# Kernel tuning notes

Measured on AMD Instinct MI355X. Metric: run time of the kernel, lower is better.

The kernel has to match this reference:

```python
import jax, jax.numpy as jnp
import numpy as np
from jax import lax

B, S, D, T = 64, 256, 1024, 60
HIST = 20  # last-20 window of attn / decoder-state history


def setup_inputs() -> dict:
    key = jax.random.key(0)
    ks = jax.random.split(key, 8)
    e_outputs = jax.random.normal(ks[0], (B, S, D), jnp.float32)
    queries = jax.random.normal(ks[1], (B, T, D), jnp.float32)
    # attention weights over source frames: rows sum to 1
    attns = jax.nn.softmax(jax.random.normal(ks[2], (B, T, S), jnp.float32), axis=-1)
    g = 0.02
    Wr = jax.random.normal(ks[3], (D, 1), jnp.float32) * g
    br = jnp.zeros((1,), jnp.float32)
    Wa = jax.random.normal(ks[4], (D, 1), jnp.float32) * g
    ba = jnp.zeros((1,), jnp.float32)
    Wq = jax.random.normal(ks[5], (D, D), jnp.float32) / np.sqrt(D)
    Wn = jax.random.normal(ks[6], (2 * D, 1), jnp.float32) * g
    bn = jnp.zeros((1,), jnp.float32)
    return {"e_outputs": e_outputs, "queries": queries, "attns": attns,
            "Wr": Wr, "br": br, "Wa": Wa, "ba": ba, "Wq": Wq, "Wn": Wn, "bn": bn}


def reference(e_outputs, queries, attns, Wr, br, Wa, ba, Wq, Wn, bn):
    Bn, Sn, Dn = e_outputs.shape
    # decay1[i] = (i+1)/20 ; decay2[i] = 1-(i+1)/50, zero-padded past 50 frames
    decay1 = (jnp.arange(HIST, dtype=jnp.float32) + 1.0) / 20.0
    idx = jnp.arange(Sn, dtype=jnp.float32)
    add0 = jnp.where(idx < 50, 1.0 - (idx + 1.0) / 50.0, 0.0)
    add_state0 = add0[None, :, None]                       # [1,S,1]
    mem0 = e_outputs * add_state0                          # [B,S,D]
    abuf0 = jnp.zeros((HIST, Bn, Sn), e_outputs.dtype)
    qbuf0 = jnp.zeros((HIST, Bn, Dn), e_outputs.dtype)

    def step(carry, x):
        mem, add_state, abuf, qbuf, i = carry
        attn_i, q_i = x                                    # [B,S], [B,D]
        # read: selected frame before memory update
        sel = jnp.einsum('bs,bsd->bd', attn_i, mem)
        # roll history buffers (newest at slot HIST-1)
        abuf = jnp.concatenate([abuf[1:], attn_i[None]], axis=0)
        qbuf = jnp.concatenate([qbuf[1:], q_i[None]], axis=0)
        k = jnp.minimum(i + 1, HIST)
        valid = jnp.arange(HIST) >= (HIST - k)
        temp = jax.nn.softmax(jnp.where(valid, decay1, -jnp.inf))
        attn_w = jnp.einsum('t,tbs->bs', temp, abuf)       # decayed attn sum
        query_s = jnp.einsum('t,tbd->bd', temp, qbuf)      # decayed query sum
        remove_prob = jax.nn.sigmoid(q_i @ Wr + br)[:, :, None]   # [B,1,1]
        add_prob = jax.nn.sigmoid(q_i @ Wa + ba)[:, :, None]      # [B,1,1]
        sim = jax.nn.sigmoid(jnp.einsum('bsd,bd->bs', mem, query_s @ Wq))[..., None]
        mem = mem * (1.0 - remove_prob * attn_w[..., None] * sim)
        last_ctx = jnp.einsum('bs,bsd->bd', attn_w, e_outputs)[:, None, :]
        cat = jnp.concatenate([e_outputs, jnp.broadcast_to(last_ctx, e_outputs.shape)], axis=-1)
        nxt = jax.nn.sigmoid(cat @ Wn + bn)                # [B,S,1]
        mem = mem + e_outputs * (1.0 - add_state) * (add_prob * nxt)
        add_state = add_state + (1.0 - add_state) * (add_prob * nxt)
        return (mem, add_state, abuf, qbuf, i + 1), sel

    init = (mem0, jnp.broadcast_to(add_state0, (Bn, Sn, 1)), abuf0, qbuf0, jnp.int32(0))
    xs = (attns.transpose(1, 0, 2), queries.transpose(1, 0, 2))
    _, sels = lax.scan(step, init, xs)
    return sels.transpose(1, 0, 2)                         # [B,T,D]
```

## Files before the change

### kernel.cpp

```cpp
#include <hip/hip_runtime.h>
#include <math.h>


#define Bn 64
#define Sn 256
#define Dn 1024
#define Tn 60
#define HISTn 20
#define LDK 72
#define K05 1.0512710963760241f
#define EINV 0.36787944117144233f

typedef __bf16 bf16x8 __attribute__((ext_vector_type(8)));
typedef float f32x4 __attribute__((ext_vector_type(4)));
typedef unsigned short us8 __attribute__((ext_vector_type(8)));

typedef const __attribute__((address_space(1))) unsigned int* gas_u32p;
typedef __attribute__((address_space(3))) unsigned int* las_u32p;

__device__ __forceinline__ void gl16(const unsigned short* g, unsigned short* l){
  __builtin_amdgcn_global_load_lds((gas_u32p)g, (las_u32p)l, 16, 0, 0);
}

__device__ __forceinline__ unsigned short f2bf(float f){
  unsigned int x; __builtin_memcpy(&x,&f,4);
  unsigned int lsb = (x >> 16) & 1u;
  x += 0x7fffu + lsb;
  return (unsigned short)(x >> 16);
}
__device__ __forceinline__ float sigmoidf_(float x){ return 1.0f/(1.0f+expf(-x)); }

__global__ __launch_bounds__(256) void conv_fused(
    const float* __restrict__ Q, const float* __restrict__ Wr,
    const float* __restrict__ br, const float* __restrict__ Wa,
    const float* __restrict__ ba, const float* __restrict__ Wq,
    const float* __restrict__ E, const float* __restrict__ Wn,
    float* __restrict__ rp, float* __restrict__ ap,
    unsigned short* __restrict__ Qbf, unsigned short* __restrict__ WT,
    unsigned short* __restrict__ Ebf,
    float* __restrict__ eW1, float* __restrict__ eW2)
{
  int tid = threadIdx.x;
  int bx = blockIdx.x;
  if (bx < Bn*Tn){
    int row = bx;
    float4 x = ((const float4*)(Q + (size_t)row*Dn))[tid];
    float4 a = ((const float4*)Wr)[tid];
    float4 b = ((const float4*)Wa)[tid];
    unsigned short o[4] = {f2bf(x.x), f2bf(x.y), f2bf(x.z), f2bf(x.w)};
    *(uint2*)&Qbf[(size_t)row*Dn + tid*4] = *(uint2*)o;
    float s1 = x.x*a.x + x.y*a.y + x.z*a.z + x.w*a.w;
    float s2 = x.x*b.x + x.y*b.y + x.z*b.z + x.w*b.w;
    for (int off = 32; off; off >>= 1){
      s1 += __shfl_down(s1, off, 64);
      s2 += __shfl_down(s2, off, 64);
    }
    __shared__ float r1[4], r2[4];
    int lane = tid & 63, wv = tid >> 6;
    if (lane == 0){ r1[wv] = s1; r2[wv] = s2; }
    __syncthreads();
    if (tid == 0){
      rp[row] = sigmoidf_(r1[0]+r1[1]+r1[2]+r1[3] + br[0]);
      ap[row] = sigmoidf_(r2[0]+r2[1]+r2[2]+r2[3] + ba[0]);
    }
  } else if (bx < Bn*Tn + 256){
    __shared__ __align__(16) unsigned short Tt[64][LDK];
    int t = bx - Bn*Tn;
    int n0 = (t >> 4)*64, k0 = (t & 15)*64;
    int kl = tid >> 4, nl4 = (tid & 15)*4;
    #pragma unroll
    for (int it = 0; it < 4; it++){
      int k = kl + it*16;
      float4 v = *(const float4*)&Wq[(size_t)(k0+k)*Dn + n0 + nl4];
      Tt[nl4+0][k] = f2bf(v.x); Tt[nl4+1][k] = f2bf(v.y);
      Tt[nl4+2][k] = f2bf(v.z); Tt[nl4+3][k] = f2bf(v.w);
    }
    __syncthreads();
    int nr = tid >> 2, kg = (tid & 3)*16;
    *(us8*)&WT[(size_t)(n0+nr)*Dn + k0+kg]   = *(us8*)&Tt[nr][kg];
    *(us8*)&WT[(size_t)(n0+nr)*Dn + k0+kg+8] = *(us8*)&Tt[nr][kg+8];
  } else {
    int row = (bx - (Bn*Tn + 256))*4 + (tid >> 6);
    int lane = tid & 63;
    const float* er = E + (size_t)row*Dn;
    unsigned short* ebr = Ebf + (size_t)row*Dn;
    float d1 = 0.f, d2 = 0.f;
    #pragma unroll
    for (int c = 0; c < 4; c++){
      int idx = c*64 + lane;
      float4 v = ((const float4*)er)[idx];
      float4 w1 = ((const float4*)Wn)[idx];
      float4 w2 = ((const float4*)(Wn + Dn))[idx];
      unsigned short o[4] = {f2bf(v.x), f2bf(v.y), f2bf(v.z), f2bf(v.w)};
      ((uint2*)ebr)[idx] = *(uint2*)o;
      d1 += v.x*w1.x + v.y*w1.y + v.z*w1.z + v.w*w1.w;
      d2 += v.x*w2.x + v.y*w2.y + v.z*w2.z + v.w*w2.w;
    }
    #pragma unroll
    for (int off = 32; off; off >>= 1){
      d1 += __shfl_down(d1, off, 64);
      d2 += __shfl_down(d2, off, 64);
    }
    if (lane == 0){ eW1[row] = d1; eW2[row] = d2; }
  }
}

__global__ __launch_bounds__(256) void gemm_qw_kr(
    const unsigned short* __restrict__ Qbf,
    const unsigned short* __restrict__ WT,
    const float* __restrict__ At,
    const float* __restrict__ eW2,
    unsigned short* __restrict__ QWbf,
    float* __restrict__ lc)
{
  int tid = threadIdx.x;
  if (blockIdx.x < (Bn*Tn/64)*(Dn/64)){
    __shared__ __align__(16) unsigned short As[64*64], Bs[64*64];
    int bx = blockIdx.x;
    int m0 = (bx >> 4) * 64, n0 = (bx & 15) * 64;
    int lane = tid & 63, wave = tid >> 6;
    int quad = lane >> 4, l16 = lane & 15;
    f32x4 acc[4];
    #pragma unroll
    for (int nt=0;nt<4;nt++)
      #pragma unroll
      for (int r=0;r<4;r++) acc[nt][r]=0.f;
    int c0 = wave*2;
    int srow = c0*8 + (lane >> 3);
    int scol = ((lane & 7) ^ (lane >> 3)) * 8;
    const unsigned short* gA0 = Qbf + (size_t)(m0 + srow)*Dn + scol;
    const unsigned short* gA1 = gA0 + 8*Dn;
    const unsigned short* gB0 = WT  + (size_t)(n0 + srow)*Dn + scol;
    const unsigned short* gB1 = gB0 + 8*Dn;
    unsigned short* lA0 = &As[c0*512];
    unsigned short* lA1 = &As[c0*512 + 512];
    unsigned short* lB0 = &Bs[c0*512];
    unsigned short* lB1 = &Bs[c0*512 + 512];
    int mrow = wave*16 + l16;
    for (int k0 = 0; k0 < Dn; k0 += 64){
      gl16(gA0 + k0, lA0);
      gl16(gA1 + k0, lA1);
      gl16(gB0 + k0, lB0);
      gl16(gB1 + k0, lB1);
      __syncthreads();
      #pragma unroll
      for (int kk = 0; kk < 2; kk++){
        bf16x8 a = *(const bf16x8*)&As[ mrow*64 + ((kk*32 + quad*8) ^ ((mrow&7)*8)) ];
        #pragma unroll
        for (int nt=0;nt<4;nt++){
          int nrow = nt*16 + l16;
          bf16x8 bb = *(const bf16x8*)&Bs[ nrow*64 + ((kk*32 + quad*8) ^ ((nrow&7)*8)) ];
          acc[nt] = __builtin_amdgcn_mfma_f32_16x16x32_bf16(a, bb, acc[nt], 0, 0, 0);
        }
      }
      __syncthreads();
    }
    #pragma unroll
    for (int nt=0;nt<4;nt++)
      #pragma unroll
      for (int r=0;r<4;r++){
        int m = m0 + wave*16 + quad*4 + r;
        int n = n0 + nt*16 + l16;
        QWbf[(size_t)m*Dn + n] = f2bf(acc[nt][r]);
      }
  } else {
    int b = blockIdx.x - (Bn*Tn/64)*(Dn/64);
    int lane = tid & 63, wv = tid >> 6;
    __shared__ float Rsh[Tn];
    float4 e2v = ((const float4*)(eW2 + (size_t)b*Sn))[lane];
    const float* at_b = At + (size_t)b*Tn*Sn;
    #pragma unroll
    for (int w = 0; w < 15; w++){
      int j = wv + w*4;
      float4 a4 = ((const float4*)(at_b + (size_t)j*Sn))[lane];
      float v = a4.x*e2v.x + a4.y*e2v.y + a4.z*e2v.z + a4.w*e2v.w;
      #pragma unroll
      for (int off = 32; off; off >>= 1) v += __shfl_down(v, off, 64);
      if (lane == 0) Rsh[j] = v;
    }
    __syncthreads();
    if (tid < Tn){
      int i = tid;
      int j0 = (i - HISTn + 1 > 0) ? i - HISTn + 1 : 0;
      float num = 0.f, den = 0.f;
      float wj = 1.f;
      for (int j = 0; j <= i; j++){
        wj *= K05;
        if (j >= j0){ num += wj * Rsh[j]; den += wj; }
      }
      lc[b*Tn + i] = num / den;
    }
  }
}

__global__ __launch_bounds__(256) void g_scan(
    const unsigned short* __restrict__ QWbf,
    const unsigned short* __restrict__ Ebf,
    const float* __restrict__ At,
    const float* __restrict__ rp,
    const float* __restrict__ ap,
    const float* __restrict__ eW1,
    const float* __restrict__ lc,
    const float* __restrict__ bnp,
    unsigned short* __restrict__ Pbf)
{
  __shared__ __align__(16) unsigned short As[64][LDK], Bs[64][LDK];
  __shared__ __align__(16) float AtL[Tn][64], GL[Tn][64];
  __shared__ float lcs[Tn], rps[Tn], aps[Tn];
  int b = blockIdx.x, s0 = blockIdx.y * 64;
  int tid = threadIdx.x, lane = tid & 63, wave = tid >> 6;
  int quad = lane >> 4, l16 = lane & 15;

  const float* at_b = At + (size_t)b*Tn*Sn + s0;
  #pragma unroll
  for (int it = 0; it < 4; it++){
    int r = it*16 + (tid >> 4);
    if (r < Tn){
      int c4 = (tid & 15)*4;
      *(float4*)&AtL[r][c4] = *(const float4*)&at_b[(size_t)r*Sn + c4];
    }
  }
  if (tid < Tn){
    lcs[tid] = lc[b*Tn + tid];
    rps[tid] = rp[b*Tn + tid];
    aps[tid] = ap[b*Tn + tid];
  }

  f32x4 acc[4];
  #pragma unroll
  for (int nt=0;nt<4;nt++)
    #pragma unroll
    for (int r=0;r<4;r++) acc[nt][r]=0.f;
  int sr = tid >> 2, sk = (tid & 3)*16;
  const unsigned short* aRow = QWbf + ((size_t)(b*Tn + sr))*Dn;
  const unsigned short* bRow = Ebf  + ((size_t)(b*Sn + s0 + sr))*Dn;
  for (int k0 = 0; k0 < Dn; k0 += 64){
    if (sr < Tn){
      *(us8*)&As[sr][sk]   = *(const us8*)&aRow[k0+sk];
      *(us8*)&As[sr][sk+8] = *(const us8*)&aRow[k0+sk+8];
    } else {
      us8 z = (us8)0;
      *(us8*)&As[sr][sk] = z; *(us8*)&As[sr][sk+8] = z;
    }
    *(us8*)&Bs[sr][sk]   = *(const us8*)&bRow[k0+sk];
    *(us8*)&Bs[sr][sk+8] = *(const us8*)&bRow[k0+sk+8];
    __syncthreads();
    #pragma unroll
    for (int kk = 0; kk < 64; kk += 32){
      bf16x8 a = *(const bf16x8*)&As[wave*16 + l16][kk + quad*8];
      #pragma unroll
      for (int nt=0;nt<4;nt++){
        bf16x8 bb = *(const bf16x8*)&Bs[nt*16 + l16][kk + quad*8];
        acc[nt] = __builtin_amdgcn_mfma_f32_16x16x32_bf16(a, bb, acc[nt], 0, 0, 0);
      }
    }
    __syncthreads();
  }
  #pragma unroll
  for (int nt=0;nt<4;nt++)
    #pragma unroll
    for (int r=0;r<4;r++){
      int t = wave*16 + quad*4 + r;
      if (t < Tn) GL[t][nt*16 + l16] = acc[nt][r];
    }
  __syncthreads();

  if (tid < 64){
    int s = s0 + tid;
    float M = (s < 50) ? (1.0f - (s+1)/50.0f) : 0.0f;
    float A = M;
    float bnv = bnp[0];
    float e1 = eW1[b*Sn + s];
    unsigned short* P_b = Pbf + (size_t)b*Tn*Sn + s;
    float num_a = 0.f, num_q = 0.f, den = 0.f, wi = 1.f;
    #pragma unroll
    for (int i = 0; i < Tn; i++){
      wi *= K05;
      float a_new = AtL[i][tid];
      float g_new = GL[i][tid];
      num_a += wi * a_new;
      num_q += wi * g_new;
      den   += wi;
      if (i >= HISTn){
        float wo = wi * EINV;
        num_a -= wo * AtL[i-HISTn][tid];
        num_q -= wo * GL[i-HISTn][tid];
        den   -= wo;
      }
      float inv = 1.0f / den;
      float aw = num_a * inv;
      float qd = num_q * inv;
      P_b[(size_t)i*Sn] = f2bf(a_new * M);
      float sim = sigmoidf_(M * qd);
      float nxt = sigmoidf_(e1 + lcs[i] + bnv);
      M = M * (1.0f - rps[i] * aw * sim);
      float g = (1.0f - A) * aps[i] * nxt;
      M += g; A += g;
    }
  }
}

__global__ __launch_bounds__(256) void gemm_sels(
    const unsigned short* __restrict__ Pbf,
    const unsigned short* __restrict__ Ebf,
    float* __restrict__ out)
{
  __shared__ __align__(16) unsigned short As[64][LDK], Bs[64][LDK];
  int b = blockIdx.x, n0 = blockIdx.y*64;
  int tid = threadIdx.x, lane = tid & 63, wave = tid >> 6;
  int quad = lane >> 4, l16 = lane & 15;
  f32x4 acc[4];
  #pragma unroll
  for (int nt=0;nt<4;nt++)
    #pragma unroll
    for (int r=0;r<4;r++) acc[nt][r]=0.f;
  int sr = tid >> 2, sk = (tid & 3)*16;
  for (int k0 = 0; k0 < Sn; k0 += 64){
    if (sr < Tn){
      *(us8*)&As[sr][sk]   = *(const us8*)&Pbf[((size_t)(b*Tn + sr))*Sn + k0+sk];
      *(us8*)&As[sr][sk+8] = *(const us8*)&Pbf[((size_t)(b*Tn + sr))*Sn + k0+sk+8];
    } else {
      us8 z = (us8)0;
      *(us8*)&As[sr][sk] = z; *(us8*)&As[sr][sk+8] = z;
    }
    {
      const unsigned short* ep = &Ebf[((size_t)(b*Sn + k0 + sr))*Dn + n0 + sk];
      us8 e0 = *(const us8*)ep;
      us8 e1 = *(const us8*)(ep + 8);
      #pragma unroll
      for (int j=0;j<8;j++){
        Bs[sk+j][sr]   = e0[j];
        Bs[sk+8+j][sr] = e1[j];
      }
    }
    __syncthreads();
    #pragma unroll
    for (int kk = 0; kk < 64; kk += 32){
      bf16x8 a = *(const bf16x8*)&As[wave*16 + l16][kk + quad*8];
      #pragma unroll
      for (int nt=0;nt<4;nt++){
        bf16x8 bb = *(const bf16x8*)&Bs[nt*16 + l16][kk + quad*8];
        acc[nt] = __builtin_amdgcn_mfma_f32_16x16x32_bf16(a, bb, acc[nt], 0, 0, 0);
      }
    }
    __syncthreads();
  }
  #pragma unroll
  for (int nt=0;nt<4;nt++)
    #pragma unroll
    for (int r=0;r<4;r++){
      int t = wave*16 + quad*4 + r;
      int d = n0 + nt*16 + l16;
      if (t < Tn) out[((size_t)(b*Tn + t))*Dn + d] = acc[nt][r];
    }
}

extern "C" void kernel_launch(void* const* d_in, const int* in_sizes, int n_in,
                              void* d_out, int out_size, void* d_ws, size_t ws_size,
                              hipStream_t stream)
{
  const float* E  = (const float*)d_in[0];
  const float* Q  = (const float*)d_in[1];
  const float* At = (const float*)d_in[2];
  const float* Wr = (const float*)d_in[3];
  const float* br = (const float*)d_in[4];
  const float* Wa = (const float*)d_in[5];
  const float* ba = (const float*)d_in[6];
  const float* Wq = (const float*)d_in[7];
  const float* Wn = (const float*)d_in[8];
  const float* bnp= (const float*)d_in[9];

  char* ws = (char*)d_ws;
  float* rp  = (float*)ws; ws += (size_t)Bn*Tn*4;
  float* ap  = (float*)ws; ws += (size_t)Bn*Tn*4;
  float* eW1 = (float*)ws; ws += (size_t)Bn*Sn*4;
  float* eW2 = (float*)ws; ws += (size_t)Bn*Sn*4;
  float* lcb = (float*)ws; ws += (size_t)Bn*Tn*4;
  unsigned short* Qbf  = (unsigned short*)ws; ws += (size_t)Bn*Tn*Dn*2;
  unsigned short* WT   = (unsigned short*)ws; ws += (size_t)Dn*Dn*2;
  unsigned short* QWbf = (unsigned short*)ws; ws += (size_t)Bn*Tn*Dn*2;
  unsigned short* Ebf  = (unsigned short*)ws; ws += (size_t)Bn*Sn*Dn*2;
  unsigned short* Pbf = (unsigned short*)ws; ws += (size_t)Bn*Tn*Sn*2;

  conv_fused<<<Bn*Tn + 256 + Bn*Sn/4, 256, 0, stream>>>(
      Q, Wr, br, Wa, ba, Wq, E, Wn, rp, ap, Qbf, WT, Ebf, eW1, eW2);
  gemm_qw_kr<<<(Bn*Tn/64)*(Dn/64) + Bn, 256, 0, stream>>>(
      Qbf, WT, At, eW2, QWbf, lcb);
  g_scan<<<dim3(Bn, Sn/64), 256, 0, stream>>>(
      QWbf, Ebf, At, rp, ap, eW1, lcb, bnp, Pbf);
  gemm_sels<<<dim3(Bn, Dn/64), 256, 0, stream>>>(Pbf, Ebf, (float*)d_out);
}
```

Measured before the change: 193.3 us.

## Double-buffer LDS tiles in all three GEMM kernels and swizzle block order

Converts the k-loops of gemm_qw_kr, g_scan and gemm_sels to double-buffered LDS tiles, so the global loads for the next tile are issued while MFMAs run on the current one. The register-staged kernels hold the prefetched tile in registers, and the async global_load_lds kernel writes straight into the alternate buffer. It also remaps block IDs in the QW GEMM so neighbouring blocks spread across different M tiles, which is meant to improve cache locality. In exchange LDS use doubles and register pressure rises, which may lower occupancy.

```diff
diff --git a/kernel.cpp b/kernel.cpp
--- a/kernel.cpp
+++ b/kernel.cpp
@@ -115,8 +115,9 @@
 {
   int tid = threadIdx.x;
   if (blockIdx.x < (Bn*Tn/64)*(Dn/64)){
-    __shared__ __align__(16) unsigned short As[64*64], Bs[64*64];
-    int bx = blockIdx.x;
+    __shared__ __align__(16) unsigned short As0_[64*64], Bs0_[64*64];
+    __shared__ __align__(16) unsigned short As1_[64*64], Bs1_[64*64];
+    int bx = (blockIdx.x & 7)*120 + (blockIdx.x >> 3);
     int m0 = (bx >> 4) * 64, n0 = (bx & 15) * 64;
     int lane = tid & 63, wave = tid >> 6;
     int quad = lane >> 4, l16 = lane & 15;
@@ -132,29 +133,39 @@
     const unsigned short* gA1 = gA0 + 8*Dn;
     const unsigned short* gB0 = WT  + (size_t)(n0 + srow)*Dn + scol;
     const unsigned short* gB1 = gB0 + 8*Dn;
-    unsigned short* lA0 = &As[c0*512];
-    unsigned short* lA1 = &As[c0*512 + 512];
-    unsigned short* lB0 = &Bs[c0*512];
-    unsigned short* lB1 = &Bs[c0*512 + 512];
     int mrow = wave*16 + l16;
-    for (int k0 = 0; k0 < Dn; k0 += 64){
-      gl16(gA0 + k0, lA0);
-      gl16(gA1 + k0, lA1);
-      gl16(gB0 + k0, lB0);
-      gl16(gB1 + k0, lB1);
+
+    #define STAGE_QW(K, A_, B_) { \
+      gl16(gA0 + (K), &A_[c0*512]);       \
+      gl16(gA1 + (K), &A_[c0*512 + 512]); \
+      gl16(gB0 + (K), &B_[c0*512]);       \
+      gl16(gB1 + (K), &B_[c0*512 + 512]); }
+    #define COMP_QW(A_, B_) { \
+      _Pragma("unroll") \
+      for (int kk = 0; kk < 2; kk++){ \
+        bf16x8 a = *(const bf16x8*)&A_[ mrow*64 + ((kk*32 + quad*8) ^ ((mrow&7)*8)) ]; \
+        _Pragma("unroll") \
+        for (int nt=0;nt<4;nt++){ \
+          int nrow = nt*16 + l16; \
+          bf16x8 bb = *(const bf16x8*)&B_[ nrow*64 + ((kk*32 + quad*8) ^ ((nrow&7)*8)) ]; \
+          acc[nt] = __builtin_amdgcn_mfma_f32_16x16x32_bf16(a, bb, acc[nt], 0, 0, 0); \
+        } \
+      } }
+
+    STAGE_QW(0, As0_, Bs0_);
+    __syncthreads();
+    #pragma unroll
+    for (int k0 = 0; k0 < Dn; k0 += 128){
+      STAGE_QW(k0+64, As1_, Bs1_);
+      COMP_QW(As0_, Bs0_);
       __syncthreads();
-      #pragma unroll
-      for (int kk = 0; kk < 2; kk++){
-        bf16x8 a = *(const bf16x8*)&As[ mrow*64 + ((kk*32 + quad*8) ^ ((mrow&7)*8)) ];
-        #pragma unroll
-        for (int nt=0;nt<4;nt++){
-          int nrow = nt*16 + l16;
-          bf16x8 bb = *(const bf16x8*)&Bs[ nrow*64 + ((kk*32 + quad*8) ^ ((nrow&7)*8)) ];
-          acc[nt] = __builtin_amdgcn_mfma_f32_16x16x32_bf16(a, bb, acc[nt], 0, 0, 0);
-        }
-      }
+      if (k0+128 < Dn) STAGE_QW(k0+128, As0_, Bs0_);
+      COMP_QW(As1_, Bs1_);
       __syncthreads();
     }
+    #undef STAGE_QW
+    #undef COMP_QW
+
     #pragma unroll
     for (int nt=0;nt<4;nt++)
       #pragma unroll
@@ -204,7 +215,8 @@
     const float* __restrict__ bnp,
     unsigned short* __restrict__ Pbf)
 {
-  __shared__ __align__(16) unsigned short As[64][LDK], Bs[64][LDK];
+  __shared__ __align__(16) unsigned short As0_[64][LDK], Bs0_[64][LDK];
+  __shared__ __align__(16) unsigned short As1_[64][LDK], Bs1_[64][LDK];
   __shared__ __align__(16) float AtL[Tn][64], GL[Tn][64];
   __shared__ float lcs[Tn], rps[Tn], aps[Tn];
   int b = blockIdx.x, s0 = blockIdx.y * 64;
@@ -234,28 +246,42 @@
   int sr = tid >> 2, sk = (tid & 3)*16;
   const unsigned short* aRow = QWbf + ((size_t)(b*Tn + sr))*Dn;
   const unsigned short* bRow = Ebf  + ((size_t)(b*Sn + s0 + sr))*Dn;
-  for (int k0 = 0; k0 < Dn; k0 += 64){
-    if (sr < Tn){
-      *(us8*)&As[sr][sk]   = *(const us8*)&aRow[k0+sk];
-      *(us8*)&As[sr][sk+8] = *(const us8*)&aRow[k0+sk+8];
-    } else {
-      us8 z = (us8)0;
-      *(us8*)&As[sr][sk] = z; *(us8*)&As[sr][sk+8] = z;
-    }
-    *(us8*)&Bs[sr][sk]   = *(const us8*)&bRow[k0+sk];
-    *(us8*)&Bs[sr][sk+8] = *(const us8*)&bRow[k0+sk+8];
-    __syncthreads();
-    #pragma unroll
-    for (int kk = 0; kk < 64; kk += 32){
-      bf16x8 a = *(const bf16x8*)&As[wave*16 + l16][kk + quad*8];
-      #pragma unroll
-      for (int nt=0;nt<4;nt++){
-        bf16x8 bb = *(const bf16x8*)&Bs[nt*16 + l16][kk + quad*8];
-        acc[nt] = __builtin_amdgcn_mfma_f32_16x16x32_bf16(a, bb, acc[nt], 0, 0, 0);
-      }
-    }
-    __syncthreads();
-  }
+
+  #define LOADR(K, ra0, ra1, rb0, rb1) { \
+    if (sr < Tn){ ra0 = *(const us8*)&aRow[(K)+sk]; ra1 = *(const us8*)&aRow[(K)+sk+8]; } \
+    else { ra0 = (us8)0; ra1 = (us8)0; } \
+    rb0 = *(const us8*)&bRow[(K)+sk]; rb1 = *(const us8*)&bRow[(K)+sk+8]; }
+  #define STORER(A_, B_, ra0, ra1, rb0, rb1) { \
+    *(us8*)&A_[sr][sk]   = ra0; *(us8*)&A_[sr][sk+8] = ra1; \
+    *(us8*)&B_[sr][sk]   = rb0; *(us8*)&B_[sr][sk+8] = rb1; }
+  #define COMP_G(A_, B_) { \
+    _Pragma("unroll") \
+    for (int kk = 0; kk < 64; kk += 32){ \
+      bf16x8 a = *(const bf16x8*)&A_[wave*16 + l16][kk + quad*8]; \
+      _Pragma("unroll") \
+      for (int nt=0;nt<4;nt++){ \
+        bf16x8 bb = *(const bf16x8*)&B_[nt*16 + l16][kk + quad*8]; \
+        acc[nt] = __builtin_amdgcn_mfma_f32_16x16x32_bf16(a, bb, acc[nt], 0, 0, 0); \
+      } \
+    } }
+
+  us8 pa0, pa1, pb0, pb1, qa0, qa1, qb0, qb1;
+  LOADR(0, pa0, pa1, pb0, pb1);
+  STORER(As0_, Bs0_, pa0, pa1, pb0, pb1);
+  for (int k0 = 0; k0 < Dn; k0 += 128){
+    LOADR(k0+64, qa0, qa1, qb0, qb1);
+    __syncthreads();
+    COMP_G(As0_, Bs0_);
+    STORER(As1_, Bs1_, qa0, qa1, qb0, qb1);
+    if (k0+128 < Dn) LOADR(k0+128, pa0, pa1, pb0, pb1);
+    __syncthreads();
+    COMP_G(As1_, Bs1_);
+    if (k0+128 < Dn) STORER(As0_, Bs0_, pa0, pa1, pb0, pb1);
+  }
+  #undef LOADR
+  #undef STORER
+  #undef COMP_G
+
   #pragma unroll
   for (int nt=0;nt<4;nt++)
     #pragma unroll
@@ -305,7 +331,8 @@
     const unsigned short* __restrict__ Ebf,
     float* __restrict__ out)
 {
-  __shared__ __align__(16) unsigned short As[64][LDK], Bs[64][LDK];
+  __shared__ __align__(16) unsigned short As0_[64][LDK], Bs0_[64][LDK];
+  __shared__ __align__(16) unsigned short As1_[64][LDK], Bs1_[64][LDK];
   int b = blockIdx.x, n0 = blockIdx.y*64;
   int tid = threadIdx.x, lane = tid & 63, wave = tid >> 6;
   int quad = lane >> 4, l16 = lane & 15;
@@ -315,36 +342,49 @@
     #pragma unroll
     for (int r=0;r<4;r++) acc[nt][r]=0.f;
   int sr = tid >> 2, sk = (tid & 3)*16;
-  for (int k0 = 0; k0 < Sn; k0 += 64){
-    if (sr < Tn){
-      *(us8*)&As[sr][sk]   = *(const us8*)&Pbf[((size_t)(b*Tn + sr))*Sn + k0+sk];
-      *(us8*)&As[sr][sk+8] = *(const us8*)&Pbf[((size_t)(b*Tn + sr))*Sn + k0+sk+8];
-    } else {
-      us8 z = (us8)0;
-      *(us8*)&As[sr][sk] = z; *(us8*)&As[sr][sk+8] = z;
-    }
-    {
-      const unsigned short* ep = &Ebf[((size_t)(b*Sn + k0 + sr))*Dn + n0 + sk];
-      us8 e0 = *(const us8*)ep;
-      us8 e1 = *(const us8*)(ep + 8);
-      #pragma unroll
-      for (int j=0;j<8;j++){
-        Bs[sk+j][sr]   = e0[j];
-        Bs[sk+8+j][sr] = e1[j];
-      }
-    }
-    __syncthreads();
-    #pragma unroll
-    for (int kk = 0; kk < 64; kk += 32){
-      bf16x8 a = *(const bf16x8*)&As[wave*16 + l16][kk + quad*8];
-      #pragma unroll
-      for (int nt=0;nt<4;nt++){
-        bf16x8 bb = *(const bf16x8*)&Bs[nt*16 + l16][kk + quad*8];
-        acc[nt] = __builtin_amdgcn_mfma_f32_16x16x32_bf16(a, bb, acc[nt], 0, 0, 0);
-      }
-    }
-    __syncthreads();
-  }
+
+  #define SLOAD(K, ra0, ra1, re0, re1) { \
+    if (sr < Tn){ \
+      const unsigned short* pp = &Pbf[((size_t)(b*Tn + sr))*Sn + (K)+sk]; \
+      ra0 = *(const us8*)pp; ra1 = *(const us8*)(pp+8); \
+    } else { ra0 = (us8)0; ra1 = (us8)0; } \
+    const unsigned short* ep = &Ebf[((size_t)(b*Sn + (K) + sr))*Dn + n0 + sk]; \
+    re0 = *(const us8*)ep; re1 = *(const us8*)(ep + 8); }
+  #define SSTORE(A_, B_, ra0, ra1, re0, re1) { \
+    *(us8*)&A_[sr][sk]   = ra0; *(us8*)&A_[sr][sk+8] = ra1; \
+    _Pragma("unroll") \
+    for (int j=0;j<8;j++){ \
+      B_[sk+j][sr]   = re0[j]; \
+      B_[sk+8+j][sr] = re1[j]; } }
+  #define COMP_S(A_, B_) { \
+    _Pragma("unroll") \
+    for (int kk = 0; kk < 64; kk += 32){ \
+      bf16x8 a = *(const bf16x8*)&A_[wave*16 + l16][kk + quad*8]; \
+      _Pragma("unroll") \
+      for (int nt=0;nt<4;nt++){ \
+        bf16x8 bb = *(const bf16x8*)&B_[nt*16 + l16][kk + quad*8]; \
+        acc[nt] = __builtin_amdgcn_mfma_f32_16x16x32_bf16(a, bb, acc[nt], 0, 0, 0); \
+      } \
+    } }
+
+  us8 pa0, pa1, pe0, pe1, qa0, qa1, qe0, qe1;
+  SLOAD(0, pa0, pa1, pe0, pe1);
+  SSTORE(As0_, Bs0_, pa0, pa1, pe0, pe1);
+  #pragma unroll
+  for (int k0 = 0; k0 < Sn; k0 += 128){
+    SLOAD(k0+64, qa0, qa1, qe0, qe1);
+    __syncthreads();
+    COMP_S(As0_, Bs0_);
+    SSTORE(As1_, Bs1_, qa0, qa1, qe0, qe1);
+    if (k0+128 < Sn) SLOAD(k0+128, pa0, pa1, pe0, pe1);
+    __syncthreads();
+    COMP_S(As1_, Bs1_);
+    if (k0+128 < Sn) SSTORE(As0_, Bs0_, pa0, pa1, pe0, pe1);
+  }
+  #undef SLOAD
+  #undef SSTORE
+  #undef COMP_S
+
   #pragma unroll
   for (int nt=0;nt<4;nt++)
     #pragma unroll
```

Result: faster. 184.1 us (-4.8%).
